# Optimization experiments

Measured on AMD Instinct MI355X. Metric: run time of the kernel, lower is better.

Reference implementation:

```python
import jax, jax.numpy as jnp
import numpy as np

B, T, C, H = 4, 4096, 1024, 16

def setup_inputs() -> dict:
    key = jax.random.key(0)
    k1, k2, k3, k4 = jax.random.split(key, 4)
    return {
        "x": jax.random.normal(k1, (B, T, C), dtype=jnp.float32),
        "W_attn": jax.random.normal(k2, (C, C), dtype=jnp.float32) * 0.02,
        "b_attn": jnp.zeros((C,), dtype=jnp.float32),
        "W_proj": jax.random.normal(k3, (C, C), dtype=jnp.float32) * 0.02,
        "b_proj": jnp.zeros((C,), dtype=jnp.float32),
        "temp": jnp.ones((H, 1), dtype=jnp.float32),
        "n_head": H,
    }

def reference(x, W_attn, b_attn, W_proj, b_proj, temp, n_head):
    Bb, Tt, Cc = x.shape
    D = Cc // n_head
    # c_attn (torch Linear: x @ W.T + b)
    w = x @ W_attn.T + b_attn                         # (B,T,C)
    w = w.reshape(Bb, Tt, n_head, D).transpose(0, 2, 1, 3)  # (B,H,T,D)
    # F.normalize over token axis (dim=-2), eps=1e-12
    norm = jnp.maximum(jnp.sqrt(jnp.sum(w * w, axis=-2, keepdims=True)), 1e-12)
    w_normed = w / norm
    tmp = jnp.sum(w_normed ** 2, axis=-1) * temp      # (B,H,T) * (H,1) -> (B,H,T)
    Pi = jax.nn.softmax(tmp, axis=1)                  # softmax over heads
    Pi_prob = Pi / (jnp.sum(Pi, axis=-1, keepdims=True) + 1e-8)  # (B,H,T)
    dots = jnp.einsum('bht,bhtd->bhd', Pi_prob, w ** 2)          # (B,H,D)
    attn = 1.0 / (1.0 + dots)                         # (B,H,D)
    y = -(w * Pi[..., None]) * attn[:, :, None, :]    # (B,H,T,D)
    y = y.transpose(0, 2, 1, 3).reshape(Bb, Tt, Cc)
    return y @ W_proj.T + b_proj
```

## Files before the change

### kernel.cpp

```cpp
#include <hip/hip_runtime.h>
#include <hip/hip_bf16.h>

#define BB 4
#define TT 4096
#define CC 1024
#define HH 16
#define DD 64

typedef __attribute__((ext_vector_type(8))) short short8;
typedef __attribute__((ext_vector_type(8))) __bf16 bf16x8;
typedef __attribute__((ext_vector_type(4))) float f32x4;

static __device__ __forceinline__ unsigned short f2bf(float f) {
    unsigned int u = __builtin_bit_cast(unsigned int, f);
    unsigned int r = (u + 0x7FFFu + ((u >> 16) & 1u)) >> 16;
    return (unsigned short)r;
}
static __device__ __forceinline__ float bf2f(unsigned short h) {
    return __builtin_bit_cast(float, ((unsigned int)h) << 16);
}

__global__ void k_f32_to_bf16(const float* __restrict__ src,
                              unsigned short* __restrict__ dst, int n4) {
    int i = blockIdx.x * 256 + threadIdx.x;
    if (i >= n4) return;
    float4 v = ((const float4*)src)[i];
    ushort4 o;
    o.x = f2bf(v.x); o.y = f2bf(v.y); o.z = f2bf(v.z); o.w = f2bf(v.w);
    ((ushort4*)dst)[i] = o;
}

#define GBM 256
#define GBN 256
#define GBK 32

static __device__ __forceinline__ void stage_tile32(
    const unsigned short* __restrict__ Gbase, unsigned short* lbase,
    int k0, int K, int wave, int lane)
{
    #pragma unroll
    for (int q = 0; q < 2; ++q) {
        int c = (wave * 2 + q) * 64 + lane;
        int r = c >> 2;
        int j = c & 3;
        int srcj = (j - (r >> 1)) & 3;
        const unsigned short* g = Gbase + (size_t)r * K + k0 + srcj * 8;
        __builtin_amdgcn_global_load_lds(
            (const __attribute__((address_space(1))) void*)g,
            (__attribute__((address_space(3))) void*)(lbase + (wave * 2 + q) * 512),
            16, 0, 0);
    }
}

template<int MODE>
__global__ __launch_bounds__(512, 2)
void k_gemm256(const unsigned short* __restrict__ A,
               const unsigned short* __restrict__ B,
               const float* __restrict__ bias,
               void* __restrict__ Cout,
               float* __restrict__ S,
               int M, int N, int K)
{
    __shared__ unsigned short lds[4][16384];
    const int tid  = threadIdx.x;
    const int wave = tid >> 6;
    const int lane = tid & 63;
    const int wr = wave >> 2;
    const int wc = wave & 3;
    const int fr = lane & 15;
    const int hi = lane >> 4;

    const int wg  = blockIdx.x;
    const int swz = (wg & 7) * 32 + (wg >> 3);
    const int bn  = swz & 3;
    const int bm  = swz >> 2;
    const int b   = bm >> 4;

    const unsigned short* Abase = A + (size_t)(bm * GBM) * K;
    const unsigned short* Bbase = B +
        ((size_t)((MODE == 1 ? b * N : 0) + bn * GBN)) * K;

    const int nt = K / GBK;

    const int sl   = (hi + (fr >> 1)) & 3;
    const int aoff = (wr * 128 + fr) * 32 + sl * 8;
    const int boff = 8192 + (wc * 64 + fr) * 32 + sl * 8;

    f32x4 acc[8][4] = {};

    stage_tile32(Abase, lds[0],        0,       K, wave, lane);
    stage_tile32(Bbase, lds[0] + 8192, 0,       K, wave, lane);
    stage_tile32(Abase, lds[1],        GBK,     K, wave, lane);
    stage_tile32(Bbase, lds[1] + 8192, GBK,     K, wave, lane);
    stage_tile32(Abase, lds[2],        2 * GBK, K, wave, lane);
    stage_tile32(Bbase, lds[2] + 8192, 2 * GBK, K, wave, lane);
    asm volatile("s_waitcnt vmcnt(8)" ::: "memory");
    __builtin_amdgcn_s_barrier();

    for (int kt = 0; kt < nt; ++kt) {
        const unsigned short* buf = lds[kt & 3];
        unsigned short* sbuf = lds[(kt + 3) & 3];
        int k3 = kt + 3; if (k3 >= nt) k3 = nt - 1;

        short8 af0[4], bf0[4];
        #pragma unroll
        for (int i = 0; i < 4; ++i) af0[i] = *(const short8*)&buf[aoff + i * 512];
        #pragma unroll
        for (int i = 0; i < 4; ++i) bf0[i] = *(const short8*)&buf[boff + i * 512];
        stage_tile32(Abase, sbuf, k3 * GBK, K, wave, lane);
        __builtin_amdgcn_s_barrier();
        asm volatile("s_waitcnt lgkmcnt(0)" ::: "memory");
        __builtin_amdgcn_s_setprio(1);
        #pragma unroll
        for (int mi = 0; mi < 4; ++mi)
            #pragma unroll
            for (int ni = 0; ni < 4; ++ni)
                acc[mi][ni] = __builtin_amdgcn_mfma_f32_16x16x32_bf16(
                    __builtin_bit_cast(bf16x8, af0[mi]),
                    __builtin_bit_cast(bf16x8, bf0[ni]),
                    acc[mi][ni], 0, 0, 0);
        __builtin_amdgcn_s_setprio(0);
        __builtin_amdgcn_s_barrier();

        short8 af1[4];
        #pragma unroll
        for (int i = 0; i < 4; ++i) af1[i] = *(const short8*)&buf[aoff + (4 + i) * 512];
        stage_tile32(Bbase, sbuf + 8192, k3 * GBK, K, wave, lane);
        asm volatile("s_waitcnt vmcnt(8)" ::: "memory");
        __builtin_amdgcn_s_barrier();
        asm volatile("s_waitcnt lgkmcnt(0)" ::: "memory");
        __builtin_amdgcn_s_setprio(1);
        #pragma unroll
        for (int mi = 0; mi < 4; ++mi)
            #pragma unroll
            for (int ni = 0; ni < 4; ++ni)
                acc[4 + mi][ni] = __builtin_amdgcn_mfma_f32_16x16x32_bf16(
                    __builtin_bit_cast(bf16x8, af1[mi]),
                    __builtin_bit_cast(bf16x8, bf0[ni]),
                    acc[4 + mi][ni], 0, 0, 0);
        __builtin_amdgcn_s_setprio(0);
        __builtin_amdgcn_s_barrier();
    }

    __syncthreads();

    const int cg = fr;
    const int rg = hi * 4;
    float* sblk = (float*)&lds[0][0];
    if (MODE == 0) {
        if (tid < GBN) sblk[tid] = 0.f;
        __syncthreads();
    }
    float csum[4] = {};
    #pragma unroll
    for (int mi = 0; mi < 8; ++mi) {
        #pragma unroll
        for (int ni = 0; ni < 4; ++ni) {
            int col = bn * GBN + wc * 64 + ni * 16 + cg;
            float bv = bias[col];
            #pragma unroll
            for (int j = 0; j < 4; ++j) {
                int row = bm * GBM + wr * 128 + mi * 16 + rg + j;
                float v = acc[mi][ni][j] + bv;
                if (MODE == 0) {
                    ((unsigned short*)Cout)[(size_t)row * N + col] = f2bf(v);
                    csum[ni] += v * v;
                } else {
                    ((float*)Cout)[(size_t)row * N + col] = v;
                }
            }
        }
    }
    if (MODE == 0) {
        #pragma unroll
        for (int ni = 0; ni < 4; ++ni)
            atomicAdd(&sblk[wc * 64 + ni * 16 + cg], csum[ni]);
        __syncthreads();
        if (tid < GBN) atomicAdd(&S[b * CC + bn * GBN + tid], sblk[tid]);
    }
}

__global__ __launch_bounds__(256)
void k_row_softmax(unsigned short* __restrict__ w16, const float* __restrict__ S,
                   const float* __restrict__ temp,
                   float* __restrict__ dotsU, float* __restrict__ sumPi)
{
    __shared__ float dots_local[CC];
    __shared__ float sPi_local[HH];
    const int tid  = threadIdx.x;
    const int wave = tid >> 6;
    const int lane = tid & 63;
    const int bb   = blockIdx.x >> 7;
    const int tile = blockIdx.x & 127;

    for (int c = tid; c < CC; c += 256) dots_local[c] = 0.f;
    if (tid < HH) sPi_local[tid] = 0.f;
    __syncthreads();

    const int g3 = lane >> 3;
    const int li = lane & 7;

    float inv[2][8], tsc[2];
    #pragma unroll
    for (int q = 0; q < 2; ++q) {
        int c = q * 512 + lane * 8;
        const float4* sp = (const float4*)&S[bb * CC + c];
        float4 s0 = sp[0], s1 = sp[1];
        inv[q][0] = 1.f / fmaxf(s0.x, 1e-24f); inv[q][1] = 1.f / fmaxf(s0.y, 1e-24f);
        inv[q][2] = 1.f / fmaxf(s0.z, 1e-24f); inv[q][3] = 1.f / fmaxf(s0.w, 1e-24f);
        inv[q][4] = 1.f / fmaxf(s1.x, 1e-24f); inv[q][5] = 1.f / fmaxf(s1.y, 1e-24f);
        inv[q][6] = 1.f / fmaxf(s1.z, 1e-24f); inv[q][7] = 1.f / fmaxf(s1.w, 1e-24f);
        tsc[q] = temp[q * 8 + g3];
    }

    float dacc[2][8] = {};
    float sPiAcc[2] = {};

    for (int i = 0; i < 8; ++i) {
        int t = tile * 32 + wave * 8 + i;
        unsigned short* row = w16 + ((size_t)bb * TT + t) * CC;
        float wf[2][8];
        float pq[2];
        #pragma unroll
        for (int q = 0; q < 2; ++q) {
            short8 v = *(const short8*)&row[q * 512 + lane * 8];
            float s = 0.f;
            #pragma unroll
            for (int j = 0; j < 8; ++j) {
                wf[q][j] = bf2f((unsigned short)v[j]);
                s += wf[q][j] * wf[q][j] * inv[q][j];
            }
            pq[q] = s;
        }
        #pragma unroll
        for (int off = 1; off < 8; off <<= 1) {
            pq[0] += __shfl_xor(pq[0], off);
            pq[1] += __shfl_xor(pq[1], off);
        }
        pq[0] *= tsc[0]; pq[1] *= tsc[1];
        float mx = fmaxf(pq[0], pq[1]);
        mx = fmaxf(mx, __shfl_xor(mx, 8));
        mx = fmaxf(mx, __shfl_xor(mx, 16));
        mx = fmaxf(mx, __shfl_xor(mx, 32));
        float e0 = __expf(pq[0] - mx), e1 = __expf(pq[1] - mx);
        float ss = e0 + e1;
        ss += __shfl_xor(ss, 8);
        ss += __shfl_xor(ss, 16);
        ss += __shfl_xor(ss, 32);
        float rs = 1.f / ss;
        float piv[2] = { e0 * rs, e1 * rs };
        #pragma unroll
        for (int q = 0; q < 2; ++q) {
            short8 yo;
            #pragma unroll
            for (int j = 0; j < 8; ++j) {
                dacc[q][j] += piv[q] * wf[q][j] * wf[q][j];
                yo[j] = (short)f2bf(-wf[q][j] * piv[q]);
            }
            *(short8*)&row[q * 512 + lane * 8] = yo;
            if (li == 0) sPiAcc[q] += piv[q];
        }
    }

    #pragma unroll
    for (int q = 0; q < 2; ++q) {
        int c = q * 512 + lane * 8;
        #pragma unroll
        for (int j = 0; j < 8; ++j)
            atomicAdd(&dots_local[c + j], dacc[q][j]);
        if (li == 0) atomicAdd(&sPi_local[q * 8 + g3], sPiAcc[q]);
    }
    __syncthreads();
    for (int c = tid; c < CC; c += 256) atomicAdd(&dotsU[bb * CC + c], dots_local[c]);
    if (tid < HH) atomicAdd(&sumPi[bb * HH + tid], sPi_local[tid]);
}

__global__ void k_scale_wproj(const float* __restrict__ Wp,
                              const float* __restrict__ dotsU,
                              const float* __restrict__ sumPi,
                              unsigned short* __restrict__ out)
{
    int i = blockIdx.x * 256 + threadIdx.x;
    int bq  = i >> 18;
    int rem = i & 262143;
    int n   = rem >> 8;
    int cg  = (rem & 255) * 4;
    float4 wv = *(const float4*)&Wp[n * CC + cg];
    float4 du = *(const float4*)&dotsU[bq * CC + cg];
    float sp = sumPi[bq * HH + (cg >> 6)] + 1e-8f;
    float a0 = 1.f / (1.f + du.x / sp);
    float a1 = 1.f / (1.f + du.y / sp);
    float a2 = 1.f / (1.f + du.z / sp);
    float a3 = 1.f / (1.f + du.w / sp);
    ushort4 o;
    o.x = f2bf(wv.x * a0); o.y = f2bf(wv.y * a1);
    o.z = f2bf(wv.z * a2); o.w = f2bf(wv.w * a3);
    *(ushort4*)&out[((size_t)bq * CC + n) * CC + cg] = o;
}

extern "C" void kernel_launch(void* const* d_in, const int* in_sizes, int n_in,
                              void* d_out, int out_size, void* d_ws, size_t ws_size,
                              hipStream_t stream) {
    const float* x      = (const float*)d_in[0];
    const float* W_attn = (const float*)d_in[1];
    const float* b_attn = (const float*)d_in[2];
    const float* W_proj = (const float*)d_in[3];
    const float* b_proj = (const float*)d_in[4];
    const float* temp   = (const float*)d_in[5];

    unsigned short* xb = (unsigned short*)d_out;

    char* ws = (char*)d_ws;
    unsigned short* w16   = (unsigned short*)(ws);
    unsigned short* Wa16  = (unsigned short*)(ws + 33554432);
    unsigned short* Wp16b = (unsigned short*)(ws + 35651584);
    float* S     = (float*)(ws + 44040192);
    float* dotsU = (float*)(ws + 44056576);
    float* sumPi = (float*)(ws + 44072960);

    k_f32_to_bf16<<<dim3(16384), dim3(256), 0, stream>>>(x, xb, 4194304);
    k_f32_to_bf16<<<dim3(1024), dim3(256), 0, stream>>>(W_attn, Wa16, 262144);

    hipMemsetAsync(S, 0, 16384 + 16384 + 256, stream);

    k_gemm256<0><<<dim3(256), dim3(512), 0, stream>>>(
        xb, Wa16, b_attn, w16, S, BB * TT, CC, CC);

    k_row_softmax<<<dim3(512), dim3(256), 0, stream>>>(w16, S, temp, dotsU, sumPi);

    k_scale_wproj<<<dim3(4096), dim3(256), 0, stream>>>(W_proj, dotsU, sumPi, Wp16b);

    k_gemm256<1><<<dim3(256), dim3(512), 0, stream>>>(
        w16, Wp16b, b_proj, d_out, nullptr, BB * TT, CC, CC);
}
```

Baseline: 131.0 us.

## Fuse fp32-to-bf16 conversion of x into first GEMM's A-tile staging

Removes the separate kernel that converts x to bf16. The first GEMM now loads fp32 A tiles into registers one stage ahead, packs them to bf16 and writes them to LDS with the same swizzle, while B still uses direct global-to-LDS loads. This saves a full extra read and write of x plus one launch. In exchange it adds register pressure, VALU conversion work inside the main loop and a manual register double-buffer, and the vmcnt accounting now has to cover the extra fp32 loads.

```diff
diff --git a/kernel.cpp b/kernel.cpp
--- a/kernel.cpp
+++ b/kernel.cpp
@@ -18,6 +18,12 @@
 }
 static __device__ __forceinline__ float bf2f(unsigned short h) {
     return __builtin_bit_cast(float, ((unsigned int)h) << 16);
+}
+static __device__ __forceinline__ short8 pack8s(f32x4 a, f32x4 b) {
+    short8 r;
+    r[0]=(short)f2bf(a[0]); r[1]=(short)f2bf(a[1]); r[2]=(short)f2bf(a[2]); r[3]=(short)f2bf(a[3]);
+    r[4]=(short)f2bf(b[0]); r[5]=(short)f2bf(b[1]); r[6]=(short)f2bf(b[2]); r[7]=(short)f2bf(b[3]);
+    return r;
 }
 
 __global__ void k_f32_to_bf16(const float* __restrict__ src,
@@ -52,9 +58,62 @@
     }
 }
 
+struct ARegs { f32x4 v0, v1, v2, v3; };
+
+#define LOAD_A(S, k4_) do { \
+    const float* _p0 = aG0 + (size_t)(k4_) * GBK; \
+    const float* _p1 = aG1 + (size_t)(k4_) * GBK; \
+    (S).v0 = *(const f32x4*)_p0; (S).v1 = *(const f32x4*)(_p0 + 4); \
+    (S).v2 = *(const f32x4*)_p1; (S).v3 = *(const f32x4*)(_p1 + 4); \
+} while(0)
+
+#define WRITE_A(S, dstbuf) do { \
+    *(short8*)&(dstbuf)[c0 * 8] = pack8s((S).v0, (S).v1); \
+    *(short8*)&(dstbuf)[c1 * 8] = pack8s((S).v2, (S).v3); \
+} while(0)
+
+#define K_TILE(kt_, WS, LS) do { \
+    const int _kt = (kt_); \
+    const unsigned short* buf = lds[_kt & 3]; \
+    unsigned short* sbuf = lds[(_kt + 3) & 3]; \
+    int _k3 = _kt + 3; if (_k3 >= nt) _k3 = nt - 1; \
+    int _k4 = _kt + 4; if (_k4 >= nt) _k4 = nt - 1; \
+     \
+    short8 af0[4], bf0[4]; \
+    _Pragma("unroll") for (int i = 0; i < 4; ++i) af0[i] = *(const short8*)&buf[aoff + i * 512]; \
+    _Pragma("unroll") for (int i = 0; i < 4; ++i) bf0[i] = *(const short8*)&buf[boff + i * 512]; \
+    if (MODE == 0) { LOAD_A(LS, _k4); WRITE_A(WS, sbuf); } \
+    else           { stage_tile32(Ab16, sbuf, _k3 * GBK, K, wave, lane); } \
+    __builtin_amdgcn_s_barrier(); \
+    asm volatile("s_waitcnt lgkmcnt(0)" ::: "memory"); \
+    __builtin_amdgcn_s_setprio(1); \
+    _Pragma("unroll") for (int mi = 0; mi < 4; ++mi) \
+        _Pragma("unroll") for (int ni = 0; ni < 4; ++ni) \
+            acc[mi][ni] = __builtin_amdgcn_mfma_f32_16x16x32_bf16( \
+                __builtin_bit_cast(bf16x8, af0[mi]), \
+                __builtin_bit_cast(bf16x8, bf0[ni]), acc[mi][ni], 0, 0, 0); \
+    __builtin_amdgcn_s_setprio(0); \
+    __builtin_amdgcn_s_barrier(); \
+     \
+    short8 af1[4]; \
+    _Pragma("unroll") for (int i = 0; i < 4; ++i) af1[i] = *(const short8*)&buf[aoff + (4 + i) * 512]; \
+    stage_tile32(Bbase, sbuf + 8192, _k3 * GBK, K, wave, lane); \
+    asm volatile("s_waitcnt vmcnt(8)" ::: "memory"); \
+    __builtin_amdgcn_s_barrier(); \
+    asm volatile("s_waitcnt lgkmcnt(0)" ::: "memory"); \
+    __builtin_amdgcn_s_setprio(1); \
+    _Pragma("unroll") for (int mi = 0; mi < 4; ++mi) \
+        _Pragma("unroll") for (int ni = 0; ni < 4; ++ni) \
+            acc[4 + mi][ni] = __builtin_amdgcn_mfma_f32_16x16x32_bf16( \
+                __builtin_bit_cast(bf16x8, af1[mi]), \
+                __builtin_bit_cast(bf16x8, bf0[ni]), acc[4 + mi][ni], 0, 0, 0); \
+    __builtin_amdgcn_s_setprio(0); \
+    __builtin_amdgcn_s_barrier(); \
+} while(0)
+
 template<int MODE>
 __global__ __launch_bounds__(512, 2)
-void k_gemm256(const unsigned short* __restrict__ A,
+void k_gemm256(const void* __restrict__ Asrc,
                const unsigned short* __restrict__ B,
                const float* __restrict__ bias,
                void* __restrict__ Cout,
@@ -76,70 +135,52 @@
     const int bm  = swz >> 2;
     const int b   = bm >> 4;
 
-    const unsigned short* Abase = A + (size_t)(bm * GBM) * K;
+    const float* Af32 = (const float*)Asrc + (size_t)(bm * GBM) * K;
+    const unsigned short* Ab16 = (const unsigned short*)Asrc + (size_t)(bm * GBM) * K;
     const unsigned short* Bbase = B +
         ((size_t)((MODE == 1 ? b * N : 0) + bn * GBN)) * K;
 
     const int nt = K / GBK;
+
+    const int c0 = (wave * 2) * 64 + lane;
+    const int c1 = c0 + 64;
+    const int r0 = c0 >> 2, s0 = ((c0 & 3) - (r0 >> 1)) & 3;
+    const int r1 = c1 >> 2, s1 = ((c1 & 3) - (r1 >> 1)) & 3;
+    const float* aG0 = Af32 + (size_t)r0 * K + s0 * 8;
+    const float* aG1 = Af32 + (size_t)r1 * K + s1 * 8;
 
     const int sl   = (hi + (fr >> 1)) & 3;
     const int aoff = (wr * 128 + fr) * 32 + sl * 8;
     const int boff = 8192 + (wc * 64 + fr) * 32 + sl * 8;
 
     f32x4 acc[8][4] = {};
-
-    stage_tile32(Abase, lds[0],        0,       K, wave, lane);
-    stage_tile32(Bbase, lds[0] + 8192, 0,       K, wave, lane);
-    stage_tile32(Abase, lds[1],        GBK,     K, wave, lane);
-    stage_tile32(Bbase, lds[1] + 8192, GBK,     K, wave, lane);
-    stage_tile32(Abase, lds[2],        2 * GBK, K, wave, lane);
-    stage_tile32(Bbase, lds[2] + 8192, 2 * GBK, K, wave, lane);
-    asm volatile("s_waitcnt vmcnt(8)" ::: "memory");
-    __builtin_amdgcn_s_barrier();
-
-    for (int kt = 0; kt < nt; ++kt) {
-        const unsigned short* buf = lds[kt & 3];
-        unsigned short* sbuf = lds[(kt + 3) & 3];
-        int k3 = kt + 3; if (k3 >= nt) k3 = nt - 1;
-
-        short8 af0[4], bf0[4];
-        #pragma unroll
-        for (int i = 0; i < 4; ++i) af0[i] = *(const short8*)&buf[aoff + i * 512];
-        #pragma unroll
-        for (int i = 0; i < 4; ++i) bf0[i] = *(const short8*)&buf[boff + i * 512];
-        stage_tile32(Abase, sbuf, k3 * GBK, K, wave, lane);
-        __builtin_amdgcn_s_barrier();
+    ARegs eS, oS;
+
+    if (MODE == 0) {
+        ARegs t0, t1, t2;
+        LOAD_A(t0, 0); LOAD_A(t1, 1); LOAD_A(t2, 2);
+        stage_tile32(Bbase, lds[0] + 8192, 0,       K, wave, lane);
+        stage_tile32(Bbase, lds[1] + 8192, GBK,     K, wave, lane);
+        stage_tile32(Bbase, lds[2] + 8192, 2 * GBK, K, wave, lane);
+        WRITE_A(t0, lds[0]); WRITE_A(t1, lds[1]); WRITE_A(t2, lds[2]);
+        LOAD_A(eS, 3);
         asm volatile("s_waitcnt lgkmcnt(0)" ::: "memory");
-        __builtin_amdgcn_s_setprio(1);
-        #pragma unroll
-        for (int mi = 0; mi < 4; ++mi)
-            #pragma unroll
-            for (int ni = 0; ni < 4; ++ni)
-                acc[mi][ni] = __builtin_amdgcn_mfma_f32_16x16x32_bf16(
-                    __builtin_bit_cast(bf16x8, af0[mi]),
-                    __builtin_bit_cast(bf16x8, bf0[ni]),
-                    acc[mi][ni], 0, 0, 0);
-        __builtin_amdgcn_s_setprio(0);
-        __builtin_amdgcn_s_barrier();
-
-        short8 af1[4];
-        #pragma unroll
-        for (int i = 0; i < 4; ++i) af1[i] = *(const short8*)&buf[aoff + (4 + i) * 512];
-        stage_tile32(Bbase, sbuf + 8192, k3 * GBK, K, wave, lane);
         asm volatile("s_waitcnt vmcnt(8)" ::: "memory");
         __builtin_amdgcn_s_barrier();
-        asm volatile("s_waitcnt lgkmcnt(0)" ::: "memory");
-        __builtin_amdgcn_s_setprio(1);
-        #pragma unroll
-        for (int mi = 0; mi < 4; ++mi)
-            #pragma unroll
-            for (int ni = 0; ni < 4; ++ni)
-                acc[4 + mi][ni] = __builtin_amdgcn_mfma_f32_16x16x32_bf16(
-                    __builtin_bit_cast(bf16x8, af1[mi]),
-                    __builtin_bit_cast(bf16x8, bf0[ni]),
-                    acc[4 + mi][ni], 0, 0, 0);
-        __builtin_amdgcn_s_setprio(0);
+    } else {
+        stage_tile32(Ab16, lds[0],         0,       K, wave, lane);
+        stage_tile32(Bbase, lds[0] + 8192, 0,       K, wave, lane);
+        stage_tile32(Ab16, lds[1],         GBK,     K, wave, lane);
+        stage_tile32(Bbase, lds[1] + 8192, GBK,     K, wave, lane);
+        stage_tile32(Ab16, lds[2],         2 * GBK, K, wave, lane);
+        stage_tile32(Bbase, lds[2] + 8192, 2 * GBK, K, wave, lane);
+        asm volatile("s_waitcnt vmcnt(8)" ::: "memory");
         __builtin_amdgcn_s_barrier();
+    }
+
+    for (int ktp = 0; ktp < nt; ktp += 2) {
+        K_TILE(ktp,     eS, oS);
+        K_TILE(ktp + 1, oS, eS);
     }
 
     __syncthreads();
@@ -308,8 +349,6 @@
     const float* b_proj = (const float*)d_in[4];
     const float* temp   = (const float*)d_in[5];
 
-    unsigned short* xb = (unsigned short*)d_out;
-
     char* ws = (char*)d_ws;
     unsigned short* w16   = (unsigned short*)(ws);
     unsigned short* Wa16  = (unsigned short*)(ws + 33554432);
@@ -318,13 +357,12 @@
     float* dotsU = (float*)(ws + 44056576);
     float* sumPi = (float*)(ws + 44072960);
 
-    k_f32_to_bf16<<<dim3(16384), dim3(256), 0, stream>>>(x, xb, 4194304);
     k_f32_to_bf16<<<dim3(1024), dim3(256), 0, stream>>>(W_attn, Wa16, 262144);
 
     hipMemsetAsync(S, 0, 16384 + 16384 + 256, stream);
 
     k_gemm256<0><<<dim3(256), dim3(512), 0, stream>>>(
-        xb, Wa16, b_attn, w16, S, BB * TT, CC, CC);
+        x, Wa16, b_attn, w16, S, BB * TT, CC, CC);
 
     k_row_softmax<<<dim3(512), dim3(256), 0, stream>>>(w16, S, temp, dotsU, sumPi);
 
```

Result: no change. 129.7 us (-1.0%).

## Collapse GEMM main loop to a single barrier per k-tile

Applied to the files above, without the earlier changes.

Restructures the bf16 MFMA GEMM main loop so each k-tile waits once on global loads and passes one barrier. It then reads all eight A fragments and four B fragments from LDS, issues the A and B prefetch for tile k+3, and runs all 32 MFMAs in one block. Before, each iteration was split into two halves with four barriers and interleaved prefetches. The aim is to cut barrier stalls and give the scheduler a longer MFMA stream. The cost is more live registers for fragments, which may lower occupancy, and less interleaving of LDS reads with compute.

```diff
diff --git a/kernel.cpp b/kernel.cpp
--- a/kernel.cpp
+++ b/kernel.cpp
@@ -94,52 +94,34 @@
     stage_tile32(Bbase, lds[1] + 8192, GBK,     K, wave, lane);
     stage_tile32(Abase, lds[2],        2 * GBK, K, wave, lane);
     stage_tile32(Bbase, lds[2] + 8192, 2 * GBK, K, wave, lane);
-    asm volatile("s_waitcnt vmcnt(8)" ::: "memory");
-    __builtin_amdgcn_s_barrier();
 
     for (int kt = 0; kt < nt; ++kt) {
         const unsigned short* buf = lds[kt & 3];
         unsigned short* sbuf = lds[(kt + 3) & 3];
         int k3 = kt + 3; if (k3 >= nt) k3 = nt - 1;
 
-        short8 af0[4], bf0[4];
-        #pragma unroll
-        for (int i = 0; i < 4; ++i) af0[i] = *(const short8*)&buf[aoff + i * 512];
-        #pragma unroll
-        for (int i = 0; i < 4; ++i) bf0[i] = *(const short8*)&buf[boff + i * 512];
+        asm volatile("s_waitcnt vmcnt(8)" ::: "memory");
+        __builtin_amdgcn_s_barrier();
+
+        short8 af[8], bfr[4];
+        #pragma unroll
+        for (int i = 0; i < 4; ++i) bfr[i] = *(const short8*)&buf[boff + i * 512];
+        #pragma unroll
+        for (int i = 0; i < 8; ++i) af[i] = *(const short8*)&buf[aoff + i * 512];
+
         stage_tile32(Abase, sbuf, k3 * GBK, K, wave, lane);
-        __builtin_amdgcn_s_barrier();
-        asm volatile("s_waitcnt lgkmcnt(0)" ::: "memory");
+        stage_tile32(Bbase, sbuf + 8192, k3 * GBK, K, wave, lane);
+
         __builtin_amdgcn_s_setprio(1);
         #pragma unroll
-        for (int mi = 0; mi < 4; ++mi)
+        for (int mi = 0; mi < 8; ++mi)
             #pragma unroll
             for (int ni = 0; ni < 4; ++ni)
                 acc[mi][ni] = __builtin_amdgcn_mfma_f32_16x16x32_bf16(
-                    __builtin_bit_cast(bf16x8, af0[mi]),
-                    __builtin_bit_cast(bf16x8, bf0[ni]),
+                    __builtin_bit_cast(bf16x8, af[mi]),
+                    __builtin_bit_cast(bf16x8, bfr[ni]),
                     acc[mi][ni], 0, 0, 0);
         __builtin_amdgcn_s_setprio(0);
-        __builtin_amdgcn_s_barrier();
-
-        short8 af1[4];
-        #pragma unroll
-        for (int i = 0; i < 4; ++i) af1[i] = *(const short8*)&buf[aoff + (4 + i) * 512];
-        stage_tile32(Bbase, sbuf + 8192, k3 * GBK, K, wave, lane);
-        asm volatile("s_waitcnt vmcnt(8)" ::: "memory");
-        __builtin_amdgcn_s_barrier();
-        asm volatile("s_waitcnt lgkmcnt(0)" ::: "memory");
-        __builtin_amdgcn_s_setprio(1);
-        #pragma unroll
-        for (int mi = 0; mi < 4; ++mi)
-            #pragma unroll
-            for (int ni = 0; ni < 4; ++ni)
-                acc[4 + mi][ni] = __builtin_amdgcn_mfma_f32_16x16x32_bf16(
-                    __builtin_bit_cast(bf16x8, af1[mi]),
-                    __builtin_bit_cast(bf16x8, bf0[ni]),
-                    acc[4 + mi][ni], 0, 0, 0);
-        __builtin_amdgcn_s_setprio(0);
-        __builtin_amdgcn_s_barrier();
     }
 
     __syncthreads();
```

Result: no change. 129.8 us (-0.9%).

## Restructure GEMM pipeline to double-buffered K=64 stages with four half-steps

Applied to the files above, without the earlier changes.

Replaces the 4-deep ring of K=32 LDS buffers with a 2-deep double buffer holding K=64 per stage, split into A/B halves for two 32-wide sub-steps. Each loop iteration now runs four MFMA half-steps and issues next-stage loads interleaved between them, with vmcnt(4) waits placed before each sub-tile read. The aim is fewer loop iterations and less wait and barrier overhead per unit of K. In exchange, prefetch depth drops from three tiles ahead to one, which may expose more global memory latency. LDS footprint stays the same.

```diff
diff --git a/kernel.cpp b/kernel.cpp
--- a/kernel.cpp
+++ b/kernel.cpp
@@ -32,7 +32,6 @@
 
 #define GBM 256
 #define GBN 256
-#define GBK 32
 
 static __device__ __forceinline__ void stage_tile32(
     const unsigned short* __restrict__ Gbase, unsigned short* lbase,
@@ -61,7 +60,7 @@
                float* __restrict__ S,
                int M, int N, int K)
 {
-    __shared__ unsigned short lds[4][16384];
+    __shared__ unsigned short lds[2][4][8192];
     const int tid  = threadIdx.x;
     const int wave = tid >> 6;
     const int lane = tid & 63;
@@ -80,64 +79,90 @@
     const unsigned short* Bbase = B +
         ((size_t)((MODE == 1 ? b * N : 0) + bn * GBN)) * K;
 
-    const int nt = K / GBK;
+    const int nt = K >> 6;
 
     const int sl   = (hi + (fr >> 1)) & 3;
     const int aoff = (wr * 128 + fr) * 32 + sl * 8;
-    const int boff = 8192 + (wc * 64 + fr) * 32 + sl * 8;
+    const int boff = (wc * 64 + fr) * 32 + sl * 8;
 
     f32x4 acc[8][4] = {};
 
-    stage_tile32(Abase, lds[0],        0,       K, wave, lane);
-    stage_tile32(Bbase, lds[0] + 8192, 0,       K, wave, lane);
-    stage_tile32(Abase, lds[1],        GBK,     K, wave, lane);
-    stage_tile32(Bbase, lds[1] + 8192, GBK,     K, wave, lane);
-    stage_tile32(Abase, lds[2],        2 * GBK, K, wave, lane);
-    stage_tile32(Bbase, lds[2] + 8192, 2 * GBK, K, wave, lane);
-    asm volatile("s_waitcnt vmcnt(8)" ::: "memory");
-    __builtin_amdgcn_s_barrier();
+    stage_tile32(Abase, &lds[0][0][0], 0,  K, wave, lane);
+    stage_tile32(Bbase, &lds[0][2][0], 0,  K, wave, lane);
+    stage_tile32(Abase, &lds[0][1][0], 32, K, wave, lane);
+    stage_tile32(Bbase, &lds[0][3][0], 32, K, wave, lane);
 
     for (int kt = 0; kt < nt; ++kt) {
-        const unsigned short* buf = lds[kt & 3];
-        unsigned short* sbuf = lds[(kt + 3) & 3];
-        int k3 = kt + 3; if (k3 >= nt) k3 = nt - 1;
-
-        short8 af0[4], bf0[4];
-        #pragma unroll
-        for (int i = 0; i < 4; ++i) af0[i] = *(const short8*)&buf[aoff + i * 512];
-        #pragma unroll
-        for (int i = 0; i < 4; ++i) bf0[i] = *(const short8*)&buf[boff + i * 512];
-        stage_tile32(Abase, sbuf, k3 * GBK, K, wave, lane);
-        __builtin_amdgcn_s_barrier();
-        asm volatile("s_waitcnt lgkmcnt(0)" ::: "memory");
+        const int p = kt & 1;
+        int kn = kt + 1; if (kn >= nt) kn = nt - 1;
+        const int kb = kn << 6;
+
+        short8 af[4], bfr[4];
+
+        asm volatile("s_waitcnt vmcnt(4)" ::: "memory");
+        __builtin_amdgcn_s_barrier();
+        #pragma unroll
+        for (int i = 0; i < 4; ++i) bfr[i] = *(const short8*)&lds[p][2][boff + i * 512];
+        #pragma unroll
+        for (int i = 0; i < 4; ++i) af[i]  = *(const short8*)&lds[p][0][aoff + i * 512];
+        stage_tile32(Abase, &lds[p ^ 1][0][0], kb, K, wave, lane);
+        __builtin_amdgcn_s_barrier();
         __builtin_amdgcn_s_setprio(1);
         #pragma unroll
         for (int mi = 0; mi < 4; ++mi)
             #pragma unroll
             for (int ni = 0; ni < 4; ++ni)
                 acc[mi][ni] = __builtin_amdgcn_mfma_f32_16x16x32_bf16(
-                    __builtin_bit_cast(bf16x8, af0[mi]),
-                    __builtin_bit_cast(bf16x8, bf0[ni]),
-                    acc[mi][ni], 0, 0, 0);
+                    __builtin_bit_cast(bf16x8, af[mi]),
+                    __builtin_bit_cast(bf16x8, bfr[ni]), acc[mi][ni], 0, 0, 0);
         __builtin_amdgcn_s_setprio(0);
         __builtin_amdgcn_s_barrier();
 
-        short8 af1[4];
-        #pragma unroll
-        for (int i = 0; i < 4; ++i) af1[i] = *(const short8*)&buf[aoff + (4 + i) * 512];
-        stage_tile32(Bbase, sbuf + 8192, k3 * GBK, K, wave, lane);
-        asm volatile("s_waitcnt vmcnt(8)" ::: "memory");
-        __builtin_amdgcn_s_barrier();
-        asm volatile("s_waitcnt lgkmcnt(0)" ::: "memory");
+        #pragma unroll
+        for (int i = 0; i < 4; ++i) af[i] = *(const short8*)&lds[p][0][aoff + (4 + i) * 512];
+        stage_tile32(Bbase, &lds[p ^ 1][2][0], kb, K, wave, lane);
+        __builtin_amdgcn_s_barrier();
         __builtin_amdgcn_s_setprio(1);
         #pragma unroll
         for (int mi = 0; mi < 4; ++mi)
             #pragma unroll
             for (int ni = 0; ni < 4; ++ni)
                 acc[4 + mi][ni] = __builtin_amdgcn_mfma_f32_16x16x32_bf16(
-                    __builtin_bit_cast(bf16x8, af1[mi]),
-                    __builtin_bit_cast(bf16x8, bf0[ni]),
-                    acc[4 + mi][ni], 0, 0, 0);
+                    __builtin_bit_cast(bf16x8, af[mi]),
+                    __builtin_bit_cast(bf16x8, bfr[ni]), acc[4 + mi][ni], 0, 0, 0);
+        __builtin_amdgcn_s_setprio(0);
+        asm volatile("s_waitcnt vmcnt(4)" ::: "memory");
+        __builtin_amdgcn_s_barrier();
+
+        #pragma unroll
+        for (int i = 0; i < 4; ++i) bfr[i] = *(const short8*)&lds[p][3][boff + i * 512];
+        #pragma unroll
+        for (int i = 0; i < 4; ++i) af[i]  = *(const short8*)&lds[p][1][aoff + i * 512];
+        stage_tile32(Abase, &lds[p ^ 1][1][0], kb + 32, K, wave, lane);
+        __builtin_amdgcn_s_barrier();
+        __builtin_amdgcn_s_setprio(1);
+        #pragma unroll
+        for (int mi = 0; mi < 4; ++mi)
+            #pragma unroll
+            for (int ni = 0; ni < 4; ++ni)
+                acc[mi][ni] = __builtin_amdgcn_mfma_f32_16x16x32_bf16(
+                    __builtin_bit_cast(bf16x8, af[mi]),
+                    __builtin_bit_cast(bf16x8, bfr[ni]), acc[mi][ni], 0, 0, 0);
+        __builtin_amdgcn_s_setprio(0);
+        __builtin_amdgcn_s_barrier();
+
+        #pragma unroll
+        for (int i = 0; i < 4; ++i) af[i] = *(const short8*)&lds[p][1][aoff + (4 + i) * 512];
+        stage_tile32(Bbase, &lds[p ^ 1][3][0], kb + 32, K, wave, lane);
+        __builtin_amdgcn_s_barrier();
+        __builtin_amdgcn_s_setprio(1);
+        #pragma unroll
+        for (int mi = 0; mi < 4; ++mi)
+            #pragma unroll
+            for (int ni = 0; ni < 4; ++ni)
+                acc[4 + mi][ni] = __builtin_amdgcn_mfma_f32_16x16x32_bf16(
+                    __builtin_bit_cast(bf16x8, af[mi]),
+                    __builtin_bit_cast(bf16x8, bfr[ni]), acc[4 + mi][ni], 0, 0, 0);
         __builtin_amdgcn_s_setprio(0);
         __builtin_amdgcn_s_barrier();
     }
@@ -146,7 +171,7 @@
 
     const int cg = fr;
     const int rg = hi * 4;
-    float* sblk = (float*)&lds[0][0];
+    float* sblk = (float*)&lds[0][0][0];
     if (MODE == 0) {
         if (tid < GBN) sblk[tid] = 0.f;
         __syncthreads();
```

After: 130.5 us. Within noise of the previous version (-0.4%).
